# Kernel tuning notes

Measured on AMD Instinct MI355X. Metric: run time of the kernel, lower is better.

The kernel has to match this reference:

```python
import jax, jax.numpy as jnp
import numpy as np

EPS = 1e-5

def conv3x3(x, w, b):
    # x: [B,C,H,W], w: [O,I,3,3] -> SAME padding (pad=1)
    y = jax.lax.conv_general_dilated(x, w, (1, 1), 'SAME',
                                     dimension_numbers=('NCHW', 'OIHW', 'NCHW'))
    return y + b[None, :, None, None]

def batchnorm(x, g, b):
    # training-mode batch statistics over (B,H,W), biased variance (torch default)
    m = x.mean(axis=(0, 2, 3), keepdims=True)
    v = x.var(axis=(0, 2, 3), keepdims=True)
    return (x - m) / jnp.sqrt(v + EPS) * g[None, :, None, None] + b[None, :, None, None]

def setup_inputs() -> dict:
    key = jax.random.key(0)
    ks = jax.random.split(key, 24)
    B, Cin, Cout, T, H, W = 16, 256, 256, 256, 32, 32
    Cq = Cout // 8
    s = lambda fan: 1.0 / np.sqrt(fan)
    inp = {
        'x': jax.random.normal(ks[0], (B, Cin, H, W), jnp.float32),
        't': jax.random.normal(ks[1], (B, T), jnp.float32),
        # time_mlp: Linear(T,T) -> ReLU -> Linear(T,Cout)
        'w_t1': jax.random.normal(ks[2], (T, T), jnp.float32) * s(T),
        'b_t1': jax.random.normal(ks[3], (T,), jnp.float32) * s(T),
        'w_t2': jax.random.normal(ks[4], (Cout, T), jnp.float32) * s(T),
        'b_t2': jax.random.normal(ks[5], (Cout,), jnp.float32) * s(T),
        # convs (3x3, pad=1)
        'w_c1': jax.random.normal(ks[6], (Cout, Cin, 3, 3), jnp.float32) * s(Cin * 9),
        'b_c1': jax.random.normal(ks[7], (Cout,), jnp.float32) * s(Cin * 9),
        'w_c2': jax.random.normal(ks[8], (Cout, Cout, 3, 3), jnp.float32) * s(Cout * 9),
        'b_c2': jax.random.normal(ks[9], (Cout,), jnp.float32) * s(Cout * 9),
        'w_tr': jax.random.normal(ks[10], (Cout, Cout, 3, 3), jnp.float32) * s(Cout * 9),
        'b_tr': jax.random.normal(ks[11], (Cout,), jnp.float32) * s(Cout * 9),
        # batchnorm affine params
        'bn1_g': jnp.ones((Cout,), jnp.float32),
        'bn1_b': jnp.zeros((Cout,), jnp.float32),
        'bn2_g': jnp.ones((Cout,), jnp.float32),
        'bn2_b': jnp.zeros((Cout,), jnp.float32),
        # self-attention 1x1 convs (stored as [O,I])
        'wq': jax.random.normal(ks[12], (Cq, Cout), jnp.float32) * s(Cout),
        'bq': jax.random.normal(ks[13], (Cq,), jnp.float32) * s(Cout),
        'wk': jax.random.normal(ks[14], (Cq, Cout), jnp.float32) * s(Cout),
        'bk': jax.random.normal(ks[15], (Cq,), jnp.float32) * s(Cout),
        'wv': jax.random.normal(ks[16], (Cout, Cout), jnp.float32) * s(Cout),
        'bv': jax.random.normal(ks[17], (Cout,), jnp.float32) * s(Cout),
        # gamma is nn.Parameter(zeros(1)); use a random value so the residual branch is exercised
        'gamma': jax.random.normal(ks[18], (1,), jnp.float32),
    }
    return inp

def reference(x, t, w_t1, b_t1, w_t2, b_t2, w_c1, b_c1, w_c2, b_c2, w_tr, b_tr,
              bn1_g, bn1_b, bn2_g, bn2_b, wq, bq, wk, bk, wv, bv, gamma):
    # --- Block ---
    h = batchnorm(jax.nn.relu(conv3x3(x, w_c1, b_c1)), bn1_g, bn1_b)
    te = jax.nn.relu(t @ w_t1.T + b_t1)
    te = jax.nn.relu(te @ w_t2.T + b_t2)          # [B, Cout]
    h = h + te[:, :, None, None]
    h = batchnorm(jax.nn.relu(conv3x3(h, w_c2, b_c2)), bn2_g, bn2_b)
    y = conv3x3(h, w_tr, b_tr)                    # transform (up=False)
    # --- SelfAttention ---
    B, C, H, W = y.shape
    yf = y.reshape(B, C, H * W)                   # [B, C, N]
    Q = jnp.einsum('qc,bcn->bnq', wq, yf) + bq[None, None, :]   # [B, N, Cq]
    K = jnp.einsum('qc,bcn->bqn', wk, yf) + bk[None, :, None]   # [B, Cq, N]
    V = jnp.einsum('vc,bcn->bvn', wv, yf) + bv[None, :, None]   # [B, C, N]
    attn = jax.nn.softmax(jnp.einsum('bnq,bqm->bnm', Q, K), axis=-1)  # [B, N, N]
    out = jnp.einsum('bcm,bnm->bcn', V, attn).reshape(B, C, H, W)
    return gamma[0] * out + y
```

## Files before the change

kernel.cpp:

```cpp
#include <hip/hip_runtime.h>
#include <hip/hip_bf16.h>

using bf16 = __hip_bfloat16;

typedef __attribute__((ext_vector_type(8))) short bf16x8_t;
typedef __attribute__((ext_vector_type(4))) float f32x4_t;

__device__ __forceinline__ float b2f(bf16 x){ return __bfloat162float(x); }
__device__ __forceinline__ bf16  f2b(float x){ return __float2bfloat16(x); }
__device__ __forceinline__ unsigned short f2bu(float x){ bf16 h = __float2bfloat16(x); return *(unsigned short*)&h; }
__device__ __forceinline__ float bits2f(unsigned int lo16){ return __uint_as_float(lo16 << 16); }

__device__ __forceinline__ void gload16(const void* g, void* l) {
    __builtin_amdgcn_global_load_lds(
        (const __attribute__((address_space(1))) unsigned int*)g,
        (__attribute__((address_space(3))) unsigned int*)l, 16, 0, 0);
}


__global__ __launch_bounds__(256) void prep_all_k(
    const float* __restrict__ x, bf16* __restrict__ Xp0, bf16* __restrict__ Xp1,
    float* __restrict__ sums,
    const float* __restrict__ t, const float* __restrict__ w_t1, const float* __restrict__ b_t1,
    const float* __restrict__ w_t2, const float* __restrict__ b_t2, float* __restrict__ te,
    const float* __restrict__ w1, const float* __restrict__ w2, const float* __restrict__ w3,
    bf16* __restrict__ W1, bf16* __restrict__ W2, bf16* __restrict__ W3o,
    const float* __restrict__ wq, const float* __restrict__ wk, const float* __restrict__ wv,
    bf16* __restrict__ WQK, bf16* __restrict__ WVb)
{
    __shared__ char smem[64 * 65 * 4];
    const int blk = blockIdx.x;
    const int tid = threadIdx.x;

    if (blk < 1024) {
        float (*xs)[65] = (float(*)[65])smem;
        if (blk == 0) {
            sums[tid] = 0.f; sums[tid + 256] = 0.f; sums[tid + 512] = 0.f; sums[tid + 768] = 0.f;
        }
        const int b = blk >> 6, ct = (blk >> 4) & 3, nt = blk & 15;
        const int c0 = ct << 6, n0 = nt << 6;
        {
            const int cl = tid >> 2, nc = (tid & 3) << 4;
            const float* src = x + (size_t)((b << 8) + c0 + cl) * 1024 + n0 + nc;
            #pragma unroll
            for (int j = 0; j < 16; j += 4) {
                const float4 v = *(const float4*)(src + j);
                xs[cl][nc + j] = v.x; xs[cl][nc + j + 1] = v.y;
                xs[cl][nc + j + 2] = v.z; xs[cl][nc + j + 3] = v.w;
            }
        }
        __syncthreads();
        {
            const int nl = tid >> 2, cc = (tid & 3) << 4;
            const int n = n0 + nl;
            const int p = ((n >> 5) + 1) * 34 + (n & 31) + 1;
            unsigned int u[8];
            #pragma unroll
            for (int k = 0; k < 8; ++k)
                u[k] = (unsigned int)f2bu(xs[cc + 2 * k][nl]) | ((unsigned int)f2bu(xs[cc + 2 * k + 1][nl]) << 16);
            bf16* dst = Xp0 + (size_t)(b * 1156 + p) * 256 + c0 + cc;
            *(uint4*)dst = make_uint4(u[0], u[1], u[2], u[3]);
            *(uint4*)(dst + 8) = make_uint4(u[4], u[5], u[6], u[7]);
        }
    } else if (blk < 1792) {
        float* ls = (float*)smem;
        const int id = blk - 1024;
        const int co = id & 255;
        const int sel = id >> 8;
        const float* w = (sel == 0) ? w1 : (sel == 1) ? w2 : w3;
        bf16* dst = (sel == 0) ? W1 : (sel == 1) ? W2 : W3o;
        const float* src = w + (size_t)co * 2304;
        #pragma unroll
        for (int i = 0; i < 9; ++i) ls[tid + (i << 8)] = src[tid + (i << 8)];
        __syncthreads();
        #pragma unroll
        for (int off = 0; off < 9; ++off)
            dst[(size_t)(co * 9 + off) * 256 + tid] = f2b(ls[tid * 9 + off]);
    } else if (blk < 2112) {
        const int r = blk - 1792;
        if (r < 32)       WQK[r * 256 + tid] = f2b(wq[r * 256 + tid]);
        else if (r < 64)  WQK[r * 256 + tid] = f2b(wk[(r - 32) * 256 + tid]);
        else              WVb[(r - 64) * 256 + tid] = f2b(wv[(r - 64) * 256 + tid]);
    } else if (blk < 2128) {
        float* tr = (float*)smem;
        float* hid = tr + 256;
        const int b = blk - 2112, j = tid;
        tr[j] = t[(b << 8) + j];
        __syncthreads();
        float s = b_t1[j];
        const float* wp = w_t1 + j * 256;
        for (int k = 0; k < 256; ++k) s += tr[k] * wp[k];
        hid[j] = fmaxf(s, 0.f);
        __syncthreads();
        float s2 = b_t2[j];
        const float* wp2 = w_t2 + j * 256;
        for (int k = 0; k < 256; ++k) s2 += hid[k] * wp2[k];
        te[(b << 8) + j] = fmaxf(s2, 0.f);
    } else {
        const int idx = (blk - 2128) * 256 + tid;
        const int v = idx >> 6;
        const int o = (idx & 63) << 1;
        if (v < 4224) {
            const int buf = v / 2112;
            const int rem = v - buf * 2112;
            const int b = rem / 132;
            const int h = rem - b * 132;
            int p;
            if (h < 34)        p = h;
            else if (h < 68)   p = 1122 + (h - 34);
            else if (h < 100)  p = (h - 68 + 1) * 34;
            else               p = (h - 100 + 1) * 34 + 33;
            unsigned int* dst = (unsigned int*)((buf ? Xp1 : Xp0) + (size_t)(b * 1156 + p) * 256);
            dst[o] = 0u; dst[o + 1] = 0u;
        }
    }
}

template<bool RELU, bool STATS>
__global__ __launch_bounds__(512, 1) void conv_mfma_k(
    const bf16* __restrict__ Xp, const bf16* __restrict__ W3,
    const float* __restrict__ bias, bf16* __restrict__ outp, float* __restrict__ sums)
{
    __shared__ bf16 Als[2][16384];
    __shared__ bf16 Bls[3][8192];
    __shared__ float sstat[256];
    const int tid = threadIdx.x;
    const int wid = tid >> 6, lane = tid & 63;
    const int wm = wid >> 2, wn = wid & 3;
    const int blk = blockIdx.x;
    const int xc = blk & 7, tt = blk >> 3;
    const int b = xc + ((tt >> 4) << 3);
    const int tile = tt & 15, mt = tile >> 1, nt = tile & 1;
    const int m0 = mt << 7, co0 = nt << 7;

    if (STATS && tid < 256) sstat[tid] = 0.f;

    const bf16* xsl = Xp + (size_t)(b * 1156 + mt * 136) * 256;

    const int lrow = tid >> 3;
    const int sL8 = (((tid & 7) ^ (lrow & 7)) << 3);
    const bf16* bgp[2];
    #pragma unroll
    for (int i = 0; i < 2; ++i)
        bgp[i] = W3 + (size_t)(co0 + (i << 6) + lrow) * 2304 + sL8;

    const int apix = (wid << 3) + (lane >> 3);
    const int aj0 = lane & 7;

    const int rsel = lane & 15, lg = lane >> 4;
    const int s0 = ((lg ^ (lane & 7)) << 3);
    const int s1 = (((lg + 4) ^ (lane & 7)) << 3);
    const int bbase = ((wn << 5) + rsel) << 6;
    int dbase[4];
    #pragma unroll
    for (int mi = 0; mi < 4; ++mi)
        dbase[mi] = ((wm << 1) + (mi >> 1)) * 34 + ((mi & 1) << 4) + rsel;

    f32x4_t acc[4][2];
    #pragma unroll
    for (int mi = 0; mi < 4; ++mi)
        #pragma unroll
        for (int ni = 0; ni < 2; ++ni)
            acc[mi][ni] = (f32x4_t){0.f, 0.f, 0.f, 0.f};

    auto STAGE_A = [&](int cic, int buf) {
        #pragma unroll
        for (int i = 0; i < 4; ++i) {
            const int pix = (i << 6) + apix;
            const int j = aj0 ^ (pix & 7);
            gload16(xsl + (size_t)pix * 256 + (cic << 6) + (j << 3),
                    &Als[buf][((i << 9) + (wid << 6)) << 3]);
        }
    };
    auto STAGE_B = [&](int st, int buf) {
        const int koff = ((st % 9) << 8) + ((st / 9) << 6);
        #pragma unroll
        for (int i = 0; i < 2; ++i)
            gload16(bgp[i] + koff, &Bls[buf][((i << 6) + (wid << 3)) << 6]);
    };

    STAGE_A(0, 0);
    STAGE_B(0, 0);
    STAGE_B(1, 1);

    #pragma unroll
    for (int st = 0; st < 36; ++st) {
        if (st < 35) asm volatile("s_waitcnt vmcnt(2)" ::: "memory");
        else         asm volatile("s_waitcnt vmcnt(0)" ::: "memory");
        __builtin_amdgcn_s_barrier();
        asm volatile("" ::: "memory");
        const int cic = st / 9, off = st % 9;
        const int doff = (off / 3) * 34 + (off % 3);
        const bf16* abuf = Als[cic & 1];
        const bf16* bbuf = Bls[st % 3];
        #pragma unroll
        for (int kh = 0; kh < 2; ++kh) {
            const int sk = kh ? s1 : s0;
            bf16x8_t av[4], bv[2];
            #pragma unroll
            for (int mi = 0; mi < 4; ++mi) {
                const int sp = dbase[mi] + doff;
                av[mi] = *(const bf16x8_t*)((const char*)abuf +
                            (sp << 7) + ((((kh << 2) + lg) ^ (sp & 7)) << 4));
            }
            #pragma unroll
            for (int ni = 0; ni < 2; ++ni)
                bv[ni] = *(const bf16x8_t*)(bbuf + bbase + (ni << 10) + sk);
            #pragma unroll
            for (int mi = 0; mi < 4; ++mi)
                #pragma unroll
                for (int ni = 0; ni < 2; ++ni)
                    acc[mi][ni] = __builtin_amdgcn_mfma_f32_16x16x32_bf16(
                        av[mi], bv[ni], acc[mi][ni], 0, 0, 0);
        }
        if (st + 2 < 36) STAGE_B(st + 2, (st + 2) % 3);
        if (off == 7 && st < 27) STAGE_A(cic + 1, (cic + 1) & 1);
    }

    const int cr = lg << 2;
    const int cc = rsel;
    #pragma unroll
    for (int ni = 0; ni < 2; ++ni) {
        const int co = co0 + (wn << 5) + (ni << 4) + cc;
        const float bb = bias[co];
        float ssum = 0.f, ssq = 0.f;
        #pragma unroll
        for (int mi = 0; mi < 4; ++mi) {
            const int n = m0 + (wm << 6) + (mi << 4) + cr;
            #pragma unroll
            for (int j = 0; j < 4; ++j) {
                float v = acc[mi][ni][j] + bb;
                if (RELU) v = fmaxf(v, 0.f);
                outp[(size_t)((b << 10) + n + j) * 256 + co] = f2b(v);
                if (STATS) { ssum += v; ssq += v * v; }
            }
        }
        if (STATS) {
            ssum += __shfl_xor(ssum, 16); ssum += __shfl_xor(ssum, 32);
            ssq  += __shfl_xor(ssq, 16);  ssq  += __shfl_xor(ssq, 32);
            if (lane < 16) {
                const int ch = (wn << 5) + (ni << 4) + cc;
                atomicAdd(&sstat[ch * 2], ssum);
                atomicAdd(&sstat[ch * 2 + 1], ssq);
            }
        }
    }
    if (STATS) {
        __syncthreads();
        if (tid < 128) {
            atomicAdd(&sums[co0 + tid], sstat[tid * 2]);
            atomicAdd(&sums[256 + co0 + tid], sstat[tid * 2 + 1]);
        }
    }
}

template<bool TE>
__global__ __launch_bounds__(256) void bn_apply_T_k(
    const bf16* __restrict__ a, const float* __restrict__ sums,
    const float* __restrict__ g, const float* __restrict__ bb,
    const float* __restrict__ te, bf16* __restrict__ Xp)
{
    const int t = threadIdx.x;
    const int row = blockIdx.x * 8 + (t >> 5);
    const int c0 = (t & 31) << 3;
    const int b = row >> 10, n = row & 1023;
    const uint4 u = *(const uint4*)(a + (size_t)row * 256 + c0);
    const unsigned int w[4] = {u.x, u.y, u.z, u.w};
    float scv[8], shv[8];
    #pragma unroll
    for (int k = 0; k < 8; ++k) {
        const int c = c0 + k;
        const float m = sums[c] * (1.f / 16384.f);
        const float var = sums[256 + c] * (1.f / 16384.f) - m * m;
        const float sc = g[c] * rsqrtf(var + 1e-5f);
        scv[k] = sc;
        shv[k] = bb[c] - m * sc + (TE ? te[(b << 8) + c] : 0.f);
    }
    unsigned int o[4];
    #pragma unroll
    for (int k = 0; k < 4; ++k) {
        const float v0 = bits2f(w[k] & 0xffffu) * scv[2*k] + shv[2*k];
        const float v1 = __uint_as_float(w[k] & 0xffff0000u) * scv[2*k+1] + shv[2*k+1];
        o[k] = (unsigned int)f2bu(v0) | ((unsigned int)f2bu(v1) << 16);
    }
    const int p = ((n >> 5) + 1) * 34 + (n & 31) + 1;
    *(uint4*)(Xp + (size_t)(b * 1156 + p) * 256 + c0) = make_uint4(o[0], o[1], o[2], o[3]);
}

__global__ __launch_bounds__(512, 1) void qkv_mfma_k(
    const bf16* __restrict__ WVb, const bf16* __restrict__ Yt,
    const float* __restrict__ bvp, bf16* __restrict__ Vb,
    const bf16* __restrict__ WQK, const float* __restrict__ bq,
    const float* __restrict__ bk, bf16* __restrict__ QKb)
{
    __shared__ bf16 Als[3][128 * 64];
    __shared__ bf16 Bls[3][128 * 64];
    const int tid = threadIdx.x;
    const int wid = tid >> 6, lane = tid & 63;

    if (blockIdx.x >= 256) {
        const int blk2 = blockIdx.x - 256;
        const int b = blk2 >> 3, m0 = (blk2 & 7) << 7;
        const int n0w = m0 + (wid << 4);
        const bf16* arow = Yt + (size_t)((b << 10) + n0w + (lane & 15)) * 256 + ((lane >> 4) << 3);
        const int boff = ((lane >> 4) << 3);
        f32x4_t acc[4];
        #pragma unroll
        for (int ni = 0; ni < 4; ++ni) acc[ni] = (f32x4_t){0.f,0.f,0.f,0.f};
        for (int k0 = 0; k0 < 256; k0 += 32) {
            const bf16x8_t av = *(const bf16x8_t*)(arow + k0);
            #pragma unroll
            for (int ni = 0; ni < 4; ++ni) {
                const bf16x8_t bv = *(const bf16x8_t*)(WQK + (ni * 16 + (lane & 15)) * 256 + k0 + boff);
                acc[ni] = __builtin_amdgcn_mfma_f32_16x16x32_bf16(av, bv, acc[ni], 0, 0, 0);
            }
        }
        const int cr = (lane >> 4) << 2, cc = lane & 15;
        #pragma unroll
        for (int ni = 0; ni < 4; ++ni) {
            const int q = ni * 16 + cc;
            const float bias = (q < 32) ? bq[q] : bk[q - 32];
            #pragma unroll
            for (int j = 0; j < 4; ++j) {
                const int n = n0w + cr + j;
                QKb[(size_t)((b << 10) + n) * 64 + q] = f2b(acc[ni][j] + bias);
            }
        }
        return;
    }

    const int wm = wid >> 2, wn = wid & 3;
    const int blk = blockIdx.x;
    const int xc = blk & 7, tt = blk >> 3;
    const int b = xc + ((tt >> 4) << 3);
    const int tile = tt & 15, vt = tile >> 3, nt = tile & 7;
    const int v0 = vt << 7, n0 = nt << 7;

    const int lrow = tid >> 3;
    const int sL8 = (((tid & 7) ^ (lrow & 7)) << 3);
    const bf16* agp[2]; const bf16* bgp[2];
    #pragma unroll
    for (int i = 0; i < 2; ++i) {
        const int r = (i << 6) + lrow;
        agp[i] = WVb + (size_t)(v0 + r) * 256 + sL8;
        bgp[i] = Yt + (size_t)((b << 10) + n0 + r) * 256 + sL8;
    }
    const int rsel = lane & 15;
    const int s0 = (((lane >> 4) ^ (lane & 7)) << 3);
    const int s1 = ((((lane >> 4) + 4) ^ (lane & 7)) << 3);
    const int abase = ((wm << 6) + rsel) << 6;
    const int bbase = ((wn << 5) + rsel) << 6;

    f32x4_t acc[4][2];
    #pragma unroll
    for (int mi = 0; mi < 4; ++mi)
        #pragma unroll
        for (int ni = 0; ni < 2; ++ni)
            acc[mi][ni] = (f32x4_t){0.f,0.f,0.f,0.f};

    auto STAGE = [&](int kt2, int buf) {
        const int koff = kt2 << 6;
        #pragma unroll
        for (int i = 0; i < 2; ++i) {
            gload16(agp[i] + koff, &Als[buf][((i << 6) + (wid << 3)) << 6]);
            gload16(bgp[i] + koff, &Bls[buf][((i << 6) + (wid << 3)) << 6]);
        }
    };

    STAGE(0, 0); STAGE(1, 1);
    for (int kt = 0; kt < 4; ++kt) {
        if (kt < 3) asm volatile("s_waitcnt vmcnt(4)" ::: "memory");
        else        asm volatile("s_waitcnt vmcnt(0)" ::: "memory");
        __builtin_amdgcn_s_barrier();
        asm volatile("" ::: "memory");
        const int cur = kt % 3;
        #pragma unroll
        for (int kh = 0; kh < 2; ++kh) {
            const int sk = kh ? s1 : s0;
            bf16x8_t av[4], bv[2];
            #pragma unroll
            for (int mi = 0; mi < 4; ++mi)
                av[mi] = *(const bf16x8_t*)(&Als[cur][abase + (mi << 10) + sk]);
            #pragma unroll
            for (int ni = 0; ni < 2; ++ni)
                bv[ni] = *(const bf16x8_t*)(&Bls[cur][bbase + (ni << 10) + sk]);
            #pragma unroll
            for (int mi = 0; mi < 4; ++mi)
                #pragma unroll
                for (int ni = 0; ni < 2; ++ni)
                    acc[mi][ni] = __builtin_amdgcn_mfma_f32_16x16x32_bf16(
                        av[mi], bv[ni], acc[mi][ni], 0, 0, 0);
        }
        if (kt + 2 < 4) STAGE(kt + 2, (kt + 2) % 3);
    }

    const int cr = (lane >> 4) << 2, cc = lane & 15;
    #pragma unroll
    for (int mi = 0; mi < 4; ++mi) {
        #pragma unroll
        for (int j = 0; j < 4; ++j) {
            const int v = v0 + (wm << 6) + (mi << 4) + cr + j;
            const float bb = bvp[v];
            #pragma unroll
            for (int ni = 0; ni < 2; ++ni) {
                const int n = n0 + (wn << 5) + (ni << 4) + cc;
                Vb[(size_t)((b << 8) + v) * 1024 + n] = f2b(acc[mi][ni][j] + bb);
            }
        }
    }
}

__global__ __launch_bounds__(256) void softmax_k(
    const bf16* __restrict__ QKb, bf16* __restrict__ P, float* __restrict__ invs)
{
    const int b = blockIdx.x >> 5, n0 = (blockIdx.x & 31) << 5;
    const int tid = threadIdx.x, wid = tid >> 6, lane = tid & 63;
    const int m0w = wid << 8;
    __shared__ float wred[4][32];

    const bf16* qbase = QKb + (size_t)((b << 10) + n0) * 64;
    const int koff = (lane >> 4) << 3;
    bf16x8_t qf[2];
    #pragma unroll
    for (int nt = 0; nt < 2; ++nt)
        qf[nt] = *(const bf16x8_t*)(qbase + (nt * 16 + (lane & 15)) * 64 + koff);
    const bf16* kbase = QKb + (size_t)(b << 10) * 64 + 32;

    float mx[2] = {-3.0e38f, -3.0e38f};
    for (int mi = 0; mi < 16; ++mi) {
        const bf16x8_t kf = *(const bf16x8_t*)(kbase + (m0w + mi * 16 + (lane & 15)) * 64 + koff);
        #pragma unroll
        for (int nt = 0; nt < 2; ++nt) {
            f32x4_t s = (f32x4_t){0.f,0.f,0.f,0.f};
            s = __builtin_amdgcn_mfma_f32_16x16x32_bf16(kf, qf[nt], s, 0, 0, 0);
            mx[nt] = fmaxf(mx[nt], fmaxf(fmaxf(s[0], s[1]), fmaxf(s[2], s[3])));
        }
    }
    #pragma unroll
    for (int nt = 0; nt < 2; ++nt) {
        mx[nt] = fmaxf(mx[nt], __shfl_xor(mx[nt], 16));
        mx[nt] = fmaxf(mx[nt], __shfl_xor(mx[nt], 32));
        if (lane < 16) wred[wid][nt * 16 + lane] = mx[nt];
    }
    __syncthreads();
    float rm[2];
    #pragma unroll
    for (int nt = 0; nt < 2; ++nt) {
        const int c = nt * 16 + (lane & 15);
        rm[nt] = fmaxf(fmaxf(wred[0][c], wred[1][c]), fmaxf(wred[2][c], wred[3][c]));
    }
    __syncthreads();

    float sm[2] = {0.f, 0.f};
    for (int mi = 0; mi < 16; ++mi) {
        const bf16x8_t kf = *(const bf16x8_t*)(kbase + (m0w + mi * 16 + (lane & 15)) * 64 + koff);
        #pragma unroll
        for (int nt = 0; nt < 2; ++nt) {
            f32x4_t s = (f32x4_t){0.f,0.f,0.f,0.f};
            s = __builtin_amdgcn_mfma_f32_16x16x32_bf16(kf, qf[nt], s, 0, 0, 0);
            const float p0 = __expf(s[0] - rm[nt]);
            const float p1 = __expf(s[1] - rm[nt]);
            const float p2 = __expf(s[2] - rm[nt]);
            const float p3 = __expf(s[3] - rm[nt]);
            sm[nt] += (p0 + p1) + (p2 + p3);
            uint2 u;
            u.x = (unsigned int)f2bu(p0) | ((unsigned int)f2bu(p1) << 16);
            u.y = (unsigned int)f2bu(p2) | ((unsigned int)f2bu(p3) << 16);
            const int n = n0 + nt * 16 + (lane & 15);
            const int m = m0w + mi * 16 + ((lane >> 4) << 2);
            *(uint2*)(P + (size_t)((b << 10) + n) * 1024 + m) = u;
        }
    }
    #pragma unroll
    for (int nt = 0; nt < 2; ++nt) {
        sm[nt] += __shfl_xor(sm[nt], 16);
        sm[nt] += __shfl_xor(sm[nt], 32);
        if (lane < 16) wred[wid][nt * 16 + lane] = sm[nt];
    }
    __syncthreads();
    if (tid < 32) {
        const float total = wred[0][tid] + wred[1][tid] + wred[2][tid] + wred[3][tid];
        invs[(b << 10) + n0 + tid] = 1.f / total;
    }
}

__global__ __launch_bounds__(512, 1) void pv_mfma_k(
    const bf16* __restrict__ Vb, const bf16* __restrict__ P,
    const float* __restrict__ invs, const bf16* __restrict__ Yt,
    const float* __restrict__ gamma, float* __restrict__ out)
{
    __shared__ bf16 Als[3][128 * 64];
    __shared__ bf16 Bls[3][128 * 64];
    const int tid = threadIdx.x;
    const int wid = tid >> 6, lane = tid & 63;
    const int wm = wid >> 2, wn = wid & 3;
    const int blk = blockIdx.x;
    const int xc = blk & 7, tt = blk >> 3;
    const int b = xc + ((tt >> 4) << 3);
    const int tile = tt & 15, ct = tile >> 3, nt = tile & 7;
    const int c0 = ct << 7, n0 = nt << 7;

    const int lrow = tid >> 3;
    const int sL8 = (((tid & 7) ^ (lrow & 7)) << 3);
    const bf16* agp[2]; const bf16* bgp[2];
    #pragma unroll
    for (int i = 0; i < 2; ++i) {
        const int r = (i << 6) + lrow;
        agp[i] = Vb + (size_t)((b << 8) + c0 + r) * 1024 + sL8;
        bgp[i] = P + (size_t)((b << 10) + n0 + r) * 1024 + sL8;
    }
    const int rsel = lane & 15;
    const int s0 = (((lane >> 4) ^ (lane & 7)) << 3);
    const int s1 = ((((lane >> 4) + 4) ^ (lane & 7)) << 3);
    const int abase = ((wm << 6) + rsel) << 6;
    const int bbase = ((wn << 5) + rsel) << 6;

    f32x4_t acc[4][2];
    #pragma unroll
    for (int mi = 0; mi < 4; ++mi)
        #pragma unroll
        for (int ni = 0; ni < 2; ++ni)
            acc[mi][ni] = (f32x4_t){0.f,0.f,0.f,0.f};

    auto STAGE = [&](int kt2, int buf) {
        const int koff = kt2 << 6;
        #pragma unroll
        for (int i = 0; i < 2; ++i) {
            gload16(agp[i] + koff, &Als[buf][((i << 6) + (wid << 3)) << 6]);
            gload16(bgp[i] + koff, &Bls[buf][((i << 6) + (wid << 3)) << 6]);
        }
    };

    STAGE(0, 0); STAGE(1, 1);
    for (int kt = 0; kt < 16; ++kt) {
        if (kt < 15) asm volatile("s_waitcnt vmcnt(4)" ::: "memory");
        else         asm volatile("s_waitcnt vmcnt(0)" ::: "memory");
        __builtin_amdgcn_s_barrier();
        asm volatile("" ::: "memory");
        const int cur = kt % 3;
        #pragma unroll
        for (int kh = 0; kh < 2; ++kh) {
            const int sk = kh ? s1 : s0;
            bf16x8_t av[4], bv[2];
            #pragma unroll
            for (int mi = 0; mi < 4; ++mi)
                av[mi] = *(const bf16x8_t*)(&Als[cur][abase + (mi << 10) + sk]);
            #pragma unroll
            for (int ni = 0; ni < 2; ++ni)
                bv[ni] = *(const bf16x8_t*)(&Bls[cur][bbase + (ni << 10) + sk]);
            #pragma unroll
            for (int mi = 0; mi < 4; ++mi)
                #pragma unroll
                for (int ni = 0; ni < 2; ++ni)
                    acc[mi][ni] = __builtin_amdgcn_mfma_f32_16x16x32_bf16(
                        av[mi], bv[ni], acc[mi][ni], 0, 0, 0);
        }
        if (kt + 2 < 16) STAGE(kt + 2, (kt + 2) % 3);
    }

    const float g = gamma[0];
    const int cr = (lane >> 4) << 2, cc = lane & 15;
    #pragma unroll
    for (int ni = 0; ni < 2; ++ni) {
        const int n = n0 + (wn << 5) + (ni << 4) + cc;
        const float gi = g * invs[(b << 10) + n];
        #pragma unroll
        for (int mi = 0; mi < 4; ++mi) {
            const int c = c0 + (wm << 6) + (mi << 4) + cr;
            const bf16* yp = Yt + (size_t)((b << 10) + n) * 256 + c;
            #pragma unroll
            for (int j = 0; j < 4; ++j)
                out[(size_t)((b << 8) + c + j) * 1024 + n] = gi * acc[mi][ni][j] + b2f(yp[j]);
        }
    }
}

extern "C" void kernel_launch(void* const* d_in, const int* in_sizes, int n_in,
                              void* d_out, int out_size, void* d_ws, size_t ws_size,
                              hipStream_t stream)
{
    const float* x     = (const float*)d_in[0];
    const float* t     = (const float*)d_in[1];
    const float* w_t1  = (const float*)d_in[2];
    const float* b_t1  = (const float*)d_in[3];
    const float* w_t2  = (const float*)d_in[4];
    const float* b_t2  = (const float*)d_in[5];
    const float* w_c1  = (const float*)d_in[6];
    const float* b_c1  = (const float*)d_in[7];
    const float* w_c2  = (const float*)d_in[8];
    const float* b_c2  = (const float*)d_in[9];
    const float* w_tr  = (const float*)d_in[10];
    const float* b_tr  = (const float*)d_in[11];
    const float* bn1g  = (const float*)d_in[12];
    const float* bn1b  = (const float*)d_in[13];
    const float* bn2g  = (const float*)d_in[14];
    const float* bn2b  = (const float*)d_in[15];
    const float* wq    = (const float*)d_in[16];
    const float* bq    = (const float*)d_in[17];
    const float* wk    = (const float*)d_in[18];
    const float* bk    = (const float*)d_in[19];
    const float* wv    = (const float*)d_in[20];
    const float* bv    = (const float*)d_in[21];
    const float* gamma = (const float*)d_in[22];
    float* out = (float*)d_out;

    char* ws = (char*)d_ws;
    float* te    = (float*)(ws + 0);
    float* sums1 = (float*)(ws + 16384);
    float* sums2 = (float*)(ws + 18432);
    char* base = ws + 32768;
    bf16* W3_1 = (bf16*)(base);
    bf16* W3_2 = (bf16*)(base + 1179648);
    bf16* W3_3 = (bf16*)(base + 2359296);
    bf16* Xp0  = (bf16*)(base + 3538944);
    bf16* Xp1  = (bf16*)(base + 13008896);
    bf16* Craw = (bf16*)(base + 22478848);
    bf16* P    = (bf16*)(base);
    bf16* Yt   = (bf16*)(base + 33554432);
    bf16* QKb  = (bf16*)(base + 41943040);
    bf16* Vb   = (bf16*)(base + 44040192);
    float* invs= (float*)(base + 52428800);
    bf16* WQK  = (bf16*)(base + 52494336);
    bf16* WVb  = (bf16*)(base + 52527104);

    prep_all_k<<<3184, 256, 0, stream>>>(
        x, Xp0, Xp1, sums1,
        t, w_t1, b_t1, w_t2, b_t2, te,
        w_c1, w_c2, w_tr, W3_1, W3_2, W3_3,
        wq, wk, wv, WQK, WVb);

    conv_mfma_k<true, true><<<256, 512, 0, stream>>>(Xp0, W3_1, b_c1, Craw, sums1);
    bn_apply_T_k<true><<<2048, 256, 0, stream>>>(Craw, sums1, bn1g, bn1b, te, Xp1);

    conv_mfma_k<true, true><<<256, 512, 0, stream>>>(Xp1, W3_2, b_c2, Craw, sums2);
    bn_apply_T_k<false><<<2048, 256, 0, stream>>>(Craw, sums2, bn2g, bn2b, nullptr, Xp0);

    conv_mfma_k<false, false><<<256, 512, 0, stream>>>(Xp0, W3_3, b_tr, Yt, nullptr);

    qkv_mfma_k<<<384, 512, 0, stream>>>(WVb, Yt, bv, Vb, WQK, bq, bk, QKb);
    softmax_k<<<512, 256, 0, stream>>>(QKb, P, invs);
    pv_mfma_k<<<256, 512, 0, stream>>>(Vb, P, invs, Yt, gamma, out);
}
```

Before: 150.7 us.

## Fold batchnorm affine into next conv weights and boundary-aware per-class biases

Removes the two bn_apply passes over the full activation tensor. Each conv now writes its ReLU output straight into the padded buffer. A small kernel folds the batch-norm scale into the next conv's weights and computes per-batch, per-border-class bias terms that account for zero padding and the time embedding. This saves a full read and write of the activation twice, at the cost of a small fold kernel and a per-element class lookup in the epilogue. It also carries some bf16 rounding risk from rescaled weights.

```diff
diff --git a/kernel.cpp b/kernel.cpp
--- a/kernel.cpp
+++ b/kernel.cpp
@@ -116,10 +116,63 @@
     }
 }
 
-template<bool RELU, bool STATS>
+template<bool TE>
+__global__ __launch_bounds__(256) void bn_fold_k(
+    const float* __restrict__ sums, const float* __restrict__ g, const float* __restrict__ bb,
+    const float* __restrict__ te, const float* __restrict__ bconv,
+    bf16* __restrict__ W, float* __restrict__ bias_cls)
+{
+    __shared__ float ss[256];
+    __shared__ float SS[16][256];
+    __shared__ float Wrow[2304];
+    __shared__ float Tl[16][9];
+    const int co = blockIdx.x, ci = threadIdx.x;
+    const float m = sums[ci] * (1.f / 16384.f);
+    const float var = sums[256 + ci] * (1.f / 16384.f) - m * m;
+    const float s = g[ci] * rsqrtf(var + 1e-5f);
+    ss[ci] = s;
+    const float base = bb[ci] - m * s;
+    #pragma unroll
+    for (int b = 0; b < 16; ++b)
+        SS[b][ci] = base + (TE ? te[(b << 8) + ci] : 0.f);
+    #pragma unroll
+    for (int i = 0; i < 9; ++i)
+        Wrow[ci + (i << 8)] = b2f(W[(size_t)co * 2304 + ci + (i << 8)]);
+    __syncthreads();
+    if (ci < 144) {
+        const int b = ci / 9, off = ci % 9;
+        float acc = 0.f;
+        for (int c = 0; c < 256; ++c)
+            acc += Wrow[off * 256 + c] * SS[b][c];
+        Tl[b][off] = acc;
+    }
+    __syncthreads();
+    if (ci < 144) {
+        const int b = ci / 9, cls = ci % 9;
+        const int rp = cls / 3, cp = cls % 3;
+        float acc = bconv[co];
+        #pragma unroll
+        for (int kh = 0; kh < 3; ++kh) {
+            if ((rp == 0 && kh == 0) || (rp == 2 && kh == 2)) continue;
+            #pragma unroll
+            for (int kw = 0; kw < 3; ++kw) {
+                if ((cp == 0 && kw == 0) || (cp == 2 && kw == 2)) continue;
+                acc += Tl[b][kh * 3 + kw];
+            }
+        }
+        bias_cls[((size_t)(b << 8) + co) * 9 + cls] = acc;
+    }
+    const float sc = ss[ci];
+    #pragma unroll
+    for (int i = 0; i < 9; ++i)
+        W[(size_t)co * 2304 + ci + (i << 8)] = f2b(Wrow[ci + (i << 8)] * sc);
+}
+
+template<bool RELU, bool STATS, bool CLS, bool PAD>
 __global__ __launch_bounds__(512, 1) void conv_mfma_k(
     const bf16* __restrict__ Xp, const bf16* __restrict__ W3,
-    const float* __restrict__ bias, bf16* __restrict__ outp, float* __restrict__ sums)
+    const float* __restrict__ bias_v, const float* __restrict__ bias_cls,
+    bf16* __restrict__ outp, float* __restrict__ sums)
 {
     __shared__ bf16 Als[2][16384];
     __shared__ bf16 Bls[3][8192];
@@ -222,16 +275,31 @@
     #pragma unroll
     for (int ni = 0; ni < 2; ++ni) {
         const int co = co0 + (wn << 5) + (ni << 4) + cc;
-        const float bb = bias[co];
+        const float* bcp = CLS ? (bias_cls + ((size_t)((b << 8) + co)) * 9) : nullptr;
+        const float bb = CLS ? 0.f : bias_v[co];
         float ssum = 0.f, ssq = 0.f;
         #pragma unroll
         for (int mi = 0; mi < 4; ++mi) {
-            const int n = m0 + (wm << 6) + (mi << 4) + cr;
+            const int nb = m0 + (wm << 6) + (mi << 4) + cr;
+            const int r = nb >> 5, col0 = nb & 31;
+            const int rp3 = ((r == 0) ? 0 : ((r == 31) ? 2 : 1)) * 3;
             #pragma unroll
             for (int j = 0; j < 4; ++j) {
-                float v = acc[mi][ni][j] + bb;
+                const int col = col0 + j;
+                float v = acc[mi][ni][j];
+                if (CLS) {
+                    const int cp = (col == 0) ? 0 : ((col == 31) ? 2 : 1);
+                    v += bcp[rp3 + cp];
+                } else {
+                    v += bb;
+                }
                 if (RELU) v = fmaxf(v, 0.f);
-                outp[(size_t)((b << 10) + n + j) * 256 + co] = f2b(v);
+                if (PAD) {
+                    const int p = (r + 1) * 34 + col + 1;
+                    outp[(size_t)(b * 1156 + p) * 256 + co] = f2b(v);
+                } else {
+                    outp[(size_t)((b << 10) + nb + j) * 256 + co] = f2b(v);
+                }
                 if (STATS) { ssum += v; ssq += v * v; }
             }
         }
@@ -252,39 +320,6 @@
             atomicAdd(&sums[256 + co0 + tid], sstat[tid * 2 + 1]);
         }
     }
-}
-
-template<bool TE>
-__global__ __launch_bounds__(256) void bn_apply_T_k(
-    const bf16* __restrict__ a, const float* __restrict__ sums,
-    const float* __restrict__ g, const float* __restrict__ bb,
-    const float* __restrict__ te, bf16* __restrict__ Xp)
-{
-    const int t = threadIdx.x;
-    const int row = blockIdx.x * 8 + (t >> 5);
-    const int c0 = (t & 31) << 3;
-    const int b = row >> 10, n = row & 1023;
-    const uint4 u = *(const uint4*)(a + (size_t)row * 256 + c0);
-    const unsigned int w[4] = {u.x, u.y, u.z, u.w};
-    float scv[8], shv[8];
-    #pragma unroll
-    for (int k = 0; k < 8; ++k) {
-        const int c = c0 + k;
-        const float m = sums[c] * (1.f / 16384.f);
-        const float var = sums[256 + c] * (1.f / 16384.f) - m * m;
-        const float sc = g[c] * rsqrtf(var + 1e-5f);
-        scv[k] = sc;
-        shv[k] = bb[c] - m * sc + (TE ? te[(b << 8) + c] : 0.f);
-    }
-    unsigned int o[4];
-    #pragma unroll
-    for (int k = 0; k < 4; ++k) {
-        const float v0 = bits2f(w[k] & 0xffffu) * scv[2*k] + shv[2*k];
-        const float v1 = __uint_as_float(w[k] & 0xffff0000u) * scv[2*k+1] + shv[2*k+1];
-        o[k] = (unsigned int)f2bu(v0) | ((unsigned int)f2bu(v1) << 16);
-    }
-    const int p = ((n >> 5) + 1) * 34 + (n & 31) + 1;
-    *(uint4*)(Xp + (size_t)(b * 1156 + p) * 256 + c0) = make_uint4(o[0], o[1], o[2], o[3]);
 }
 
 __global__ __launch_bounds__(512, 1) void qkv_mfma_k(
@@ -614,7 +649,6 @@
     bf16* W3_3 = (bf16*)(base + 2359296);
     bf16* Xp0  = (bf16*)(base + 3538944);
     bf16* Xp1  = (bf16*)(base + 13008896);
-    bf16* Craw = (bf16*)(base + 22478848);
     bf16* P    = (bf16*)(base);
     bf16* Yt   = (bf16*)(base + 33554432);
     bf16* QKb  = (bf16*)(base + 41943040);
@@ -622,6 +656,8 @@
     float* invs= (float*)(base + 52428800);
     bf16* WQK  = (bf16*)(base + 52494336);
     bf16* WVb  = (bf16*)(base + 52527104);
+    float* bias_cls1 = (float*)(base + 52658176);
+    float* bias_cls2 = (float*)(base + 52805632);
 
     prep_all_k<<<3184, 256, 0, stream>>>(
         x, Xp0, Xp1, sums1,
@@ -629,13 +665,14 @@
         w_c1, w_c2, w_tr, W3_1, W3_2, W3_3,
         wq, wk, wv, WQK, WVb);
 
-    conv_mfma_k<true, true><<<256, 512, 0, stream>>>(Xp0, W3_1, b_c1, Craw, sums1);
-    bn_apply_T_k<true><<<2048, 256, 0, stream>>>(Craw, sums1, bn1g, bn1b, te, Xp1);
-
-    conv_mfma_k<true, true><<<256, 512, 0, stream>>>(Xp1, W3_2, b_c2, Craw, sums2);
-    bn_apply_T_k<false><<<2048, 256, 0, stream>>>(Craw, sums2, bn2g, bn2b, nullptr, Xp0);
-
-    conv_mfma_k<false, false><<<256, 512, 0, stream>>>(Xp0, W3_3, b_tr, Yt, nullptr);
+    conv_mfma_k<true, true, false, true><<<256, 512, 0, stream>>>(
+        Xp0, W3_1, b_c1, nullptr, Xp1, sums1);
+    bn_fold_k<true><<<256, 256, 0, stream>>>(sums1, bn1g, bn1b, te, b_c2, W3_2, bias_cls1);
+    conv_mfma_k<true, true, true, true><<<256, 512, 0, stream>>>(
+        Xp1, W3_2, nullptr, bias_cls1, Xp0, sums2);
+    bn_fold_k<false><<<256, 256, 0, stream>>>(sums2, bn2g, bn2b, nullptr, b_tr, W3_3, bias_cls2);
+    conv_mfma_k<false, false, true, false><<<256, 512, 0, stream>>>(
+        Xp0, W3_3, nullptr, bias_cls2, Yt, nullptr);
 
     qkv_mfma_k<<<384, 512, 0, stream>>>(WVb, Yt, bv, Vb, WQK, bq, bk, QKb);
     softmax_k<<<512, 256, 0, stream>>>(QKb, P, invs);
```

Measured after the change: 153.5 us. About the same (+1.9%).

## Use 4-wave blocks with 64x64 warp tiles in conv and PV GEMM kernels

Applied to the files above, without the earlier changes.

The conv and PV MFMA kernels drop from 8 waves (512 threads) to 4 waves (256 threads) per block. Each wave now computes a 64x64 output tile (4x4 MFMA fragments) instead of 64x32, so each wave reuses more fragments per LDS read. Staging loops issue twice as many 16-byte global-to-LDS loads per thread, and the vmcnt waits are retuned to match. This cuts LDS traffic per MFMA but lowers wave-level parallelism per CU with only 256 blocks and raises register pressure.

```diff
diff --git a/kernel.cpp b/kernel.cpp
--- a/kernel.cpp
+++ b/kernel.cpp
@@ -117,7 +117,7 @@
 }
 
 template<bool RELU, bool STATS>
-__global__ __launch_bounds__(512, 1) void conv_mfma_k(
+__global__ __launch_bounds__(256, 1) void conv_mfma_k(
     const bf16* __restrict__ Xp, const bf16* __restrict__ W3,
     const float* __restrict__ bias, bf16* __restrict__ outp, float* __restrict__ sums)
 {
@@ -126,57 +126,57 @@
     __shared__ float sstat[256];
     const int tid = threadIdx.x;
     const int wid = tid >> 6, lane = tid & 63;
-    const int wm = wid >> 2, wn = wid & 3;
+    const int wm = wid >> 1, wn = wid & 1;
     const int blk = blockIdx.x;
     const int xc = blk & 7, tt = blk >> 3;
     const int b = xc + ((tt >> 4) << 3);
     const int tile = tt & 15, mt = tile >> 1, nt = tile & 1;
     const int m0 = mt << 7, co0 = nt << 7;
 
-    if (STATS && tid < 256) sstat[tid] = 0.f;
+    if (STATS) sstat[tid] = 0.f;
 
     const bf16* xsl = Xp + (size_t)(b * 1156 + mt * 136) * 256;
 
-    const int lrow = tid >> 3;
-    const int sL8 = (((tid & 7) ^ (lrow & 7)) << 3);
-    const bf16* bgp[2];
-    #pragma unroll
-    for (int i = 0; i < 2; ++i)
-        bgp[i] = W3 + (size_t)(co0 + (i << 6) + lrow) * 2304 + sL8;
-
-    const int apix = (wid << 3) + (lane >> 3);
-    const int aj0 = lane & 7;
+    const int l8 = lane >> 3;
+    const int aj = ((lane & 7) ^ l8) << 3;
+    const bf16* agp[8];
+    #pragma unroll
+    for (int i = 0; i < 8; ++i)
+        agp[i] = xsl + (size_t)((i << 5) + (wid << 3) + l8) * 256 + aj;
+
+    const int brr = tid >> 3;
+    const int sL8 = (((tid & 7) ^ (brr & 7)) << 3);
+    const bf16* bgp[4];
+    #pragma unroll
+    for (int i = 0; i < 4; ++i)
+        bgp[i] = W3 + (size_t)(co0 + (i << 5) + brr) * 2304 + sL8;
 
     const int rsel = lane & 15, lg = lane >> 4;
     const int s0 = ((lg ^ (lane & 7)) << 3);
     const int s1 = (((lg + 4) ^ (lane & 7)) << 3);
-    const int bbase = ((wn << 5) + rsel) << 6;
+    const int bbase = ((wn << 6) + rsel) << 6;
     int dbase[4];
     #pragma unroll
     for (int mi = 0; mi < 4; ++mi)
         dbase[mi] = ((wm << 1) + (mi >> 1)) * 34 + ((mi & 1) << 4) + rsel;
 
-    f32x4_t acc[4][2];
+    f32x4_t acc[4][4];
     #pragma unroll
     for (int mi = 0; mi < 4; ++mi)
         #pragma unroll
-        for (int ni = 0; ni < 2; ++ni)
+        for (int ni = 0; ni < 4; ++ni)
             acc[mi][ni] = (f32x4_t){0.f, 0.f, 0.f, 0.f};
 
     auto STAGE_A = [&](int cic, int buf) {
         #pragma unroll
-        for (int i = 0; i < 4; ++i) {
-            const int pix = (i << 6) + apix;
-            const int j = aj0 ^ (pix & 7);
-            gload16(xsl + (size_t)pix * 256 + (cic << 6) + (j << 3),
-                    &Als[buf][((i << 9) + (wid << 6)) << 3]);
-        }
+        for (int i = 0; i < 8; ++i)
+            gload16(agp[i] + (cic << 6), &Als[buf][(i << 11) + (wid << 9)]);
     };
     auto STAGE_B = [&](int st, int buf) {
         const int koff = ((st % 9) << 8) + ((st / 9) << 6);
         #pragma unroll
-        for (int i = 0; i < 2; ++i)
-            gload16(bgp[i] + koff, &Bls[buf][((i << 6) + (wid << 3)) << 6]);
+        for (int i = 0; i < 4; ++i)
+            gload16(bgp[i] + koff, &Bls[buf][(i << 11) + (wid << 9)]);
     };
 
     STAGE_A(0, 0);
@@ -185,8 +185,9 @@
 
     #pragma unroll
     for (int st = 0; st < 36; ++st) {
-        if (st < 35) asm volatile("s_waitcnt vmcnt(2)" ::: "memory");
-        else         asm volatile("s_waitcnt vmcnt(0)" ::: "memory");
+        if (st == 35)           asm volatile("s_waitcnt vmcnt(0)" ::: "memory");
+        else if (st % 9 == 8)   asm volatile("s_waitcnt vmcnt(12)" ::: "memory");
+        else                    asm volatile("s_waitcnt vmcnt(4)" ::: "memory");
         __builtin_amdgcn_s_barrier();
         asm volatile("" ::: "memory");
         const int cic = st / 9, off = st % 9;
@@ -196,7 +197,7 @@
         #pragma unroll
         for (int kh = 0; kh < 2; ++kh) {
             const int sk = kh ? s1 : s0;
-            bf16x8_t av[4], bv[2];
+            bf16x8_t av[4], bv[4];
             #pragma unroll
             for (int mi = 0; mi < 4; ++mi) {
                 const int sp = dbase[mi] + doff;
@@ -204,12 +205,12 @@
                             (sp << 7) + ((((kh << 2) + lg) ^ (sp & 7)) << 4));
             }
             #pragma unroll
-            for (int ni = 0; ni < 2; ++ni)
+            for (int ni = 0; ni < 4; ++ni)
                 bv[ni] = *(const bf16x8_t*)(bbuf + bbase + (ni << 10) + sk);
             #pragma unroll
             for (int mi = 0; mi < 4; ++mi)
                 #pragma unroll
-                for (int ni = 0; ni < 2; ++ni)
+                for (int ni = 0; ni < 4; ++ni)
                     acc[mi][ni] = __builtin_amdgcn_mfma_f32_16x16x32_bf16(
                         av[mi], bv[ni], acc[mi][ni], 0, 0, 0);
         }
@@ -220,18 +221,18 @@
     const int cr = lg << 2;
     const int cc = rsel;
     #pragma unroll
-    for (int ni = 0; ni < 2; ++ni) {
-        const int co = co0 + (wn << 5) + (ni << 4) + cc;
+    for (int ni = 0; ni < 4; ++ni) {
+        const int co = co0 + (wn << 6) + (ni << 4) + cc;
         const float bb = bias[co];
         float ssum = 0.f, ssq = 0.f;
         #pragma unroll
         for (int mi = 0; mi < 4; ++mi) {
-            const int n = m0 + (wm << 6) + (mi << 4) + cr;
+            const int nb = m0 + (wm << 6) + (mi << 4) + cr;
             #pragma unroll
             for (int j = 0; j < 4; ++j) {
                 float v = acc[mi][ni][j] + bb;
                 if (RELU) v = fmaxf(v, 0.f);
-                outp[(size_t)((b << 10) + n + j) * 256 + co] = f2b(v);
+                outp[(size_t)((b << 10) + nb + j) * 256 + co] = f2b(v);
                 if (STATS) { ssum += v; ssq += v * v; }
             }
         }
@@ -239,7 +240,7 @@
             ssum += __shfl_xor(ssum, 16); ssum += __shfl_xor(ssum, 32);
             ssq  += __shfl_xor(ssq, 16);  ssq  += __shfl_xor(ssq, 32);
             if (lane < 16) {
-                const int ch = (wn << 5) + (ni << 4) + cc;
+                const int ch = (wn << 6) + (ni << 4) + cc;
                 atomicAdd(&sstat[ch * 2], ssum);
                 atomicAdd(&sstat[ch * 2 + 1], ssq);
             }
@@ -484,56 +485,57 @@
     }
 }
 
-__global__ __launch_bounds__(512, 1) void pv_mfma_k(
+__global__ __launch_bounds__(256, 1) void pv_mfma_k(
     const bf16* __restrict__ Vb, const bf16* __restrict__ P,
     const float* __restrict__ invs, const bf16* __restrict__ Yt,
     const float* __restrict__ gamma, float* __restrict__ out)
 {
-    __shared__ bf16 Als[3][128 * 64];
-    __shared__ bf16 Bls[3][128 * 64];
+    __shared__ bf16 Als[3][8192];
+    __shared__ bf16 Bls[3][8192];
     const int tid = threadIdx.x;
     const int wid = tid >> 6, lane = tid & 63;
-    const int wm = wid >> 2, wn = wid & 3;
+    const int wm = wid >> 1, wn = wid & 1;
     const int blk = blockIdx.x;
     const int xc = blk & 7, tt = blk >> 3;
     const int b = xc + ((tt >> 4) << 3);
     const int tile = tt & 15, ct = tile >> 3, nt = tile & 7;
     const int c0 = ct << 7, n0 = nt << 7;
 
-    const int lrow = tid >> 3;
-    const int sL8 = (((tid & 7) ^ (lrow & 7)) << 3);
-    const bf16* agp[2]; const bf16* bgp[2];
-    #pragma unroll
-    for (int i = 0; i < 2; ++i) {
-        const int r = (i << 6) + lrow;
+    const int brr = tid >> 3;
+    const int sL8 = (((tid & 7) ^ (brr & 7)) << 3);
+    const bf16* agp[4]; const bf16* bgp[4];
+    #pragma unroll
+    for (int i = 0; i < 4; ++i) {
+        const int r = (i << 5) + brr;
         agp[i] = Vb + (size_t)((b << 8) + c0 + r) * 1024 + sL8;
         bgp[i] = P + (size_t)((b << 10) + n0 + r) * 1024 + sL8;
     }
-    const int rsel = lane & 15;
-    const int s0 = (((lane >> 4) ^ (lane & 7)) << 3);
-    const int s1 = ((((lane >> 4) + 4) ^ (lane & 7)) << 3);
+    const int rsel = lane & 15, lg = lane >> 4;
+    const int s0 = ((lg ^ (lane & 7)) << 3);
+    const int s1 = (((lg + 4) ^ (lane & 7)) << 3);
     const int abase = ((wm << 6) + rsel) << 6;
-    const int bbase = ((wn << 5) + rsel) << 6;
-
-    f32x4_t acc[4][2];
+    const int bbase = ((wn << 6) + rsel) << 6;
+
+    f32x4_t acc[4][4];
     #pragma unroll
     for (int mi = 0; mi < 4; ++mi)
         #pragma unroll
-        for (int ni = 0; ni < 2; ++ni)
+        for (int ni = 0; ni < 4; ++ni)
             acc[mi][ni] = (f32x4_t){0.f,0.f,0.f,0.f};
 
     auto STAGE = [&](int kt2, int buf) {
         const int koff = kt2 << 6;
         #pragma unroll
-        for (int i = 0; i < 2; ++i) {
-            gload16(agp[i] + koff, &Als[buf][((i << 6) + (wid << 3)) << 6]);
-            gload16(bgp[i] + koff, &Bls[buf][((i << 6) + (wid << 3)) << 6]);
+        for (int i = 0; i < 4; ++i) {
+            gload16(agp[i] + koff, &Als[buf][(i << 11) + (wid << 9)]);
+            gload16(bgp[i] + koff, &Bls[buf][(i << 11) + (wid << 9)]);
         }
     };
 
     STAGE(0, 0); STAGE(1, 1);
+    #pragma unroll
     for (int kt = 0; kt < 16; ++kt) {
-        if (kt < 15) asm volatile("s_waitcnt vmcnt(4)" ::: "memory");
+        if (kt < 15) asm volatile("s_waitcnt vmcnt(8)" ::: "memory");
         else         asm volatile("s_waitcnt vmcnt(0)" ::: "memory");
         __builtin_amdgcn_s_barrier();
         asm volatile("" ::: "memory");
@@ -541,17 +543,17 @@
         #pragma unroll
         for (int kh = 0; kh < 2; ++kh) {
             const int sk = kh ? s1 : s0;
-            bf16x8_t av[4], bv[2];
+            bf16x8_t av[4], bv[4];
             #pragma unroll
             for (int mi = 0; mi < 4; ++mi)
                 av[mi] = *(const bf16x8_t*)(&Als[cur][abase + (mi << 10) + sk]);
             #pragma unroll
-            for (int ni = 0; ni < 2; ++ni)
+            for (int ni = 0; ni < 4; ++ni)
                 bv[ni] = *(const bf16x8_t*)(&Bls[cur][bbase + (ni << 10) + sk]);
             #pragma unroll
             for (int mi = 0; mi < 4; ++mi)
                 #pragma unroll
-                for (int ni = 0; ni < 2; ++ni)
+                for (int ni = 0; ni < 4; ++ni)
                     acc[mi][ni] = __builtin_amdgcn_mfma_f32_16x16x32_bf16(
                         av[mi], bv[ni], acc[mi][ni], 0, 0, 0);
         }
@@ -559,10 +561,10 @@
     }
 
     const float g = gamma[0];
-    const int cr = (lane >> 4) << 2, cc = lane & 15;
-    #pragma unroll
-    for (int ni = 0; ni < 2; ++ni) {
-        const int n = n0 + (wn << 5) + (ni << 4) + cc;
+    const int cr = lg << 2, cc = rsel;
+    #pragma unroll
+    for (int ni = 0; ni < 4; ++ni) {
+        const int n = n0 + (wn << 6) + (ni << 4) + cc;
         const float gi = g * invs[(b << 10) + n];
         #pragma unroll
         for (int mi = 0; mi < 4; ++mi) {
@@ -629,15 +631,15 @@
         w_c1, w_c2, w_tr, W3_1, W3_2, W3_3,
         wq, wk, wv, WQK, WVb);
 
-    conv_mfma_k<true, true><<<256, 512, 0, stream>>>(Xp0, W3_1, b_c1, Craw, sums1);
+    conv_mfma_k<true, true><<<256, 256, 0, stream>>>(Xp0, W3_1, b_c1, Craw, sums1);
     bn_apply_T_k<true><<<2048, 256, 0, stream>>>(Craw, sums1, bn1g, bn1b, te, Xp1);
 
-    conv_mfma_k<true, true><<<256, 512, 0, stream>>>(Xp1, W3_2, b_c2, Craw, sums2);
+    conv_mfma_k<true, true><<<256, 256, 0, stream>>>(Xp1, W3_2, b_c2, Craw, sums2);
     bn_apply_T_k<false><<<2048, 256, 0, stream>>>(Craw, sums2, bn2g, bn2b, nullptr, Xp0);
 
-    conv_mfma_k<false, false><<<256, 512, 0, stream>>>(Xp0, W3_3, b_tr, Yt, nullptr);
+    conv_mfma_k<false, false><<<256, 256, 0, stream>>>(Xp0, W3_3, b_tr, Yt, nullptr);
 
     qkv_mfma_k<<<384, 512, 0, stream>>>(WVb, Yt, bv, Vb, WQK, bq, bk, QKb);
     softmax_k<<<512, 256, 0, stream>>>(QKb, P, invs);
-    pv_mfma_k<<<256, 512, 0, stream>>>(Vb, P, invs, Yt, gamma, out);
-}
+    pv_mfma_k<<<256, 256, 0, stream>>>(Vb, P, invs, Yt, gamma, out);
+}
```

Measured after the change: 165.9 us (median of 3 runs). +10.1%, slower.
